# Performance work log

Measured on AMD Instinct MI355X. Metric: run time of the kernel, lower is better.

## Reference

```python
import jax, jax.numpy as jnp
import numpy as np
import math

MAX_VAL = 1e12
N = 1024        # max / actual seq len (l == n required by the module)
D = 512         # model dim
DK = 64         # head dim
H = D // DK     # 8 total heads
H_LOC = 4       # locker (local) heads
H_GLB = H - H_LOC


def setup_inputs() -> dict:
    key = jax.random.key(0)
    ks = jax.random.split(key, 10)
    b = 16
    inp = {
        "query": jax.random.normal(ks[0], (b, H, N, DK), jnp.float32),
        "key": jax.random.normal(ks[1], (b, H, N, DK), jnp.float32),
        "value": jax.random.normal(ks[2], (b, H, N, DK), jnp.float32),
        "mask": jax.random.randint(ks[3], (b, 1, N, N), 0, 2, jnp.int32),
        "users": jax.random.normal(ks[4], (b, N, D), jnp.float32),
        # learned params
        "rel_pos_table": jax.random.normal(ks[5], (2 * N - 1, H_LOC * DK), jnp.float32) * 0.02,
        "user_proj_w": jax.random.normal(ks[6], (D, H_LOC * DK), jnp.float32) * 0.02,
        "user_proj_b": jnp.zeros((H_LOC * DK,), jnp.float32),
        "mlp_w": jax.random.normal(ks[7], (H_LOC, DK), jnp.float32) * 0.1,
        "mlp_b": jnp.zeros((H_LOC,), jnp.float32),
    }
    return inp


def reference(query, key, value, mask, users, rel_pos_table, user_proj_w, user_proj_b, mlp_w, mlp_b):
    b, h, l, d_k = query.shape
    scale = 1.0 / math.sqrt(d_k)
    mask0 = (mask == 0)

    # ---- global heads: plain softmax attention ----
    q_g, k_g, v_g = query[:, :H_GLB], key[:, :H_GLB], value[:, :H_GLB]
    scores_g = jnp.einsum('bhqd,bhkd->bhqk', q_g, k_g) * scale
    scores_g = jnp.where(mask0, -MAX_VAL, scores_g)
    p_attn_g = jax.nn.softmax(scores_g, axis=-1)
    out_g = jnp.einsum('bhqk,bhkd->bhqd', p_attn_g, v_g)

    # ---- local (locker) heads: scores + per-head linear reweight ----
    q_l, k_l, v_l = query[:, H_GLB:], key[:, H_GLB:], value[:, H_GLB:]
    scores_l = jnp.einsum('bhqd,bhkd->bhqk', q_l, k_l) * scale

    # distance matrix and relative-position embedding, [h,q,k,d]
    distance = jnp.arange(l)[None, :] - jnp.arange(l)[:, None] + N - 1
    rel = rel_pos_table[distance].reshape(l, l, H_LOC, d_k).transpose(2, 0, 1, 3)

    # user projection -> [b,h,q,d]
    u = (users @ user_proj_w + user_proj_b).reshape(b, l, H_LOC, d_k).transpose(0, 2, 1, 3)

    # per-head Linear(d_k,1) applied to (rel + v_q + v_k + u_q); linearity lets us
    # distribute the dot product instead of materializing the [b,h,l,l,d_k] tensor.
    rw_rel = jnp.einsum('hqkd,hd->hqk', rel, mlp_w)[None]          # [1,h,q,k]
    rw_vq = jnp.einsum('bhqd,hd->bhq', v_l, mlp_w)[..., None]      # [b,h,q,1]
    rw_vk = jnp.einsum('bhkd,hd->bhk', v_l, mlp_w)[:, :, None, :]  # [b,h,1,k]
    rw_u = jnp.einsum('bhqd,hd->bhq', u, mlp_w)[..., None]         # [b,h,q,1]
    reweight = rw_rel + rw_vq + rw_vk + rw_u + mlp_b[None, :, None, None]

    scores_l = scores_l + reweight
    scores_l = jnp.where(mask0, -MAX_VAL, scores_l)
    p_attn_l = jax.nn.softmax(scores_l, axis=-1)
    out_l = jnp.einsum('bhqk,bhkd->bhqd', p_attn_l, v_l)

    out = jnp.concatenate([out_g, out_l], axis=1)
    return (out, p_attn_g, p_attn_l)
```

## Files before the change

kernel.cpp:

```cpp
#include <hip/hip_runtime.h>
#include <math.h>

#define NTOK 1024
#define SCALE 0.125f

#define WS_TREL   0
#define WS_RWV    8192
#define WS_RWU    73728
#define WS_W2     139264
#define WS_B2     141312

#define PG_OFF   8388608
#define PL_OFF   75497472

__global__ void prep0(const float* __restrict__ upw, const float* __restrict__ upb,
                      const float* __restrict__ mlw, const float* __restrict__ mlb,
                      const float* __restrict__ rpt, float* __restrict__ ws) {
    int gid = blockIdx.x * 256 + threadIdx.x;
    if (gid < 2048) {
        int c = gid >> 2, hl = gid & 3;
        const float* wrow = upw + c * 256 + hl * 64;
        const float* m = mlw + hl * 64;
        float acc = 0.f;
        #pragma unroll 8
        for (int d = 0; d < 64; ++d) acc += wrow[d] * m[d];
        ws[WS_W2 + gid] = acc;
    } else if (gid < 2052) {
        int hl = gid - 2048;
        const float* m = mlw + hl * 64;
        float acc = mlb[hl];
        #pragma unroll 8
        for (int d = 0; d < 64; ++d) acc += upb[hl * 64 + d] * m[d];
        ws[WS_B2 + hl] = acc;
    } else if (gid < 2052 + 2047 * 4) {
        int tt = gid - 2052;
        int dist = tt >> 2, hl = tt & 3;
        const float* r = rpt + dist * 256 + hl * 64;
        const float* m = mlw + hl * 64;
        float acc = 0.f;
        #pragma unroll 8
        for (int d = 0; d < 64; ++d) acc += r[d] * m[d];
        ws[WS_TREL + hl * 2048 + dist] = acc;
    }
}

__global__ void prep1(const float* __restrict__ value, const float* __restrict__ users,
                      const float* __restrict__ mlw, float* __restrict__ ws) {
    int t = threadIdx.x;
    int lane = t & 63, w = t >> 6;
    if (blockIdx.x < 256) {
        int wave = blockIdx.x * 4 + w;
        for (int r = 0; r < 64; ++r) {
            int row = wave * 64 + r;
            int b = row >> 12, hl = (row >> 10) & 3, n = row & 1023;
            float v = value[(((b * 8) + 4 + hl) * 1024 + n) * 64 + lane] * mlw[hl * 64 + lane];
            for (int m = 32; m; m >>= 1) v += __shfl_xor(v, m, 64);
            if (lane == 0) ws[WS_RWV + row] = v;
        }
    } else {
        __shared__ float w2[2052];
        for (int i = t; i < 2052; i += 256) w2[i] = ws[WS_W2 + i];
        __syncthreads();
        int wave = (blockIdx.x - 256) * 4 + w;
        for (int r = 0; r < 64; ++r) {
            int row = wave * 64 + r;
            int b = row >> 10, q = row & 1023;
            const float* ur = users + (b * 1024 + q) * 512;
            float p0 = 0.f, p1 = 0.f, p2 = 0.f, p3 = 0.f;
            #pragma unroll
            for (int j = 0; j < 8; ++j) {
                float uu = ur[lane + 64 * j];
                const float* wr = &w2[(lane + 64 * j) * 4];
                p0 += uu * wr[0]; p1 += uu * wr[1]; p2 += uu * wr[2]; p3 += uu * wr[3];
            }
            for (int m = 32; m; m >>= 1) {
                p0 += __shfl_xor(p0, m, 64); p1 += __shfl_xor(p1, m, 64);
                p2 += __shfl_xor(p2, m, 64); p3 += __shfl_xor(p3, m, 64);
            }
            if (lane == 0) {
                ws[WS_RWU + (b * 4 + 0) * 1024 + q] = p0 + w2[2048];
                ws[WS_RWU + (b * 4 + 1) * 1024 + q] = p1 + w2[2049];
                ws[WS_RWU + (b * 4 + 2) * 1024 + q] = p2 + w2[2050];
                ws[WS_RWU + (b * 4 + 3) * 1024 + q] = p3 + w2[2051];
            }
        }
    }
}

__launch_bounds__(256, 2)
__global__ void attn_main(const float* __restrict__ Q, const float* __restrict__ K,
                          const float* __restrict__ V, const int* __restrict__ mask,
                          const float* __restrict__ ws, float* __restrict__ out) {
    __shared__ float QT_s[64 * 128];
    __shared__ float SB[128 * 64];

    const int t = threadIdx.x;
    const int lbid = (blockIdx.x & 7) * 128 + (blockIdx.x >> 3);
    const int b = lbid >> 6, h = (lbid >> 3) & 7, qt = lbid & 7;
    const int q0 = qt * 128;
    const int qg = t >> 4, kg = t & 15;
    const bool loc = (h >= 4);
    const int hl = loc ? (h - 4) : 0;

    const float* Qb = Q + ((b * 8 + h) * 1024 + q0) * 64;
    const float* Kb = K + ((b * 8 + h) * 1024) * 64;
    const float* Vb = V + ((b * 8 + h) * 1024) * 64;
    const int*   Mb = mask + (b * 1024 + q0) * 1024;
    float* Pb = out + (loc ? (PL_OFF + ((b * 4 + hl) * 1024 + q0) * 1024)
                           : (PG_OFF + ((b * 4 + h ) * 1024 + q0) * 1024));
    float* Ob = out + ((b * 8 + h) * 1024 + q0) * 64;
    const float* rwv  = ws + WS_RWV + (b * 4 + hl) * 1024;
    const float* trel = ws + WS_TREL + hl * 2048;

    {
        int qr = t >> 1, d0 = 32 * (t & 1);
        const float* src = Qb + qr * 64 + d0;
        #pragma unroll
        for (int i = 0; i < 8; ++i) {
            float4 vv = *(const float4*)(src + 4 * i);
            QT_s[(d0 + 4 * i + 0) * 128 + qr] = vv.x;
            QT_s[(d0 + 4 * i + 1) * 128 + qr] = vv.y;
            QT_s[(d0 + 4 * i + 2) * 128 + qr] = vv.z;
            QT_s[(d0 + 4 * i + 3) * 128 + qr] = vv.w;
        }
    }
    float rq_r[8];
    #pragma unroll
    for (int i = 0; i < 8; ++i) rq_r[i] = 0.f;
    if (loc) {
        #pragma unroll
        for (int i = 0; i < 8; ++i) {
            int qq = 8 * qg + i;
            rq_r[i] = ws[WS_RWV + (b * 4 + hl) * 1024 + q0 + qq]
                    + ws[WS_RWU + (b * 4 + hl) * 1024 + q0 + qq];
        }
    }

    float o_[8][4];
    #pragma unroll
    for (int i = 0; i < 8; ++i)
        #pragma unroll
        for (int j = 0; j < 4; ++j) o_[i][j] = 0.f;
    float rs[8];
    #pragma unroll
    for (int i = 0; i < 8; ++i) rs[i] = 0.f;

    for (int s = 0; s < 8; ++s) {
        const int k0 = s * 128;
        __syncthreads();
        {
            int kr = t >> 1, d0 = 32 * (t & 1);
            const float* src = Kb + (k0 + kr) * 64 + d0;
            #pragma unroll
            for (int i = 0; i < 8; ++i) {
                float4 vv = *(const float4*)(src + 4 * i);
                SB[(d0 + 4 * i + 0) * 128 + kr] = vv.x;
                SB[(d0 + 4 * i + 1) * 128 + kr] = vv.y;
                SB[(d0 + 4 * i + 2) * 128 + kr] = vv.z;
                SB[(d0 + 4 * i + 3) * 128 + kr] = vv.w;
            }
        }
        __syncthreads();
        float c_[8][8];
        #pragma unroll
        for (int i = 0; i < 8; ++i)
            #pragma unroll
            for (int j = 0; j < 8; ++j) c_[i][j] = 0.f;
        #pragma unroll 4
        for (int d = 0; d < 64; ++d) {
            float4 a0 = *(const float4*)&QT_s[d * 128 + 8 * qg];
            float4 a1 = *(const float4*)&QT_s[d * 128 + 8 * qg + 4];
            float4 b0 = *(const float4*)&SB[d * 128 + 8 * kg];
            float4 b1 = *(const float4*)&SB[d * 128 + 8 * kg + 4];
            float aa[8] = {a0.x, a0.y, a0.z, a0.w, a1.x, a1.y, a1.z, a1.w};
            float bb[8] = {b0.x, b0.y, b0.z, b0.w, b1.x, b1.y, b1.z, b1.w};
            #pragma unroll
            for (int i = 0; i < 8; ++i)
                #pragma unroll
                for (int j = 0; j < 8; ++j)
                    c_[i][j] = fmaf(aa[i], bb[j], c_[i][j]);
        }
        float rvv[8];
        #pragma unroll
        for (int j = 0; j < 8; ++j) rvv[j] = 0.f;
        if (loc) {
            float4 rv0 = *(const float4*)(rwv + k0 + 8 * kg);
            float4 rv1 = *(const float4*)(rwv + k0 + 8 * kg + 4);
            rvv[0] = rv0.x; rvv[1] = rv0.y; rvv[2] = rv0.z; rvv[3] = rv0.w;
            rvv[4] = rv1.x; rvv[5] = rv1.y; rvv[6] = rv1.z; rvv[7] = rv1.w;
        }
        #pragma unroll
        for (int i = 0; i < 8; ++i) {
            int qq = 8 * qg + i;
            const int* mrow = Mb + qq * 1024 + k0 + 8 * kg;
            int4 m0 = *(const int4*)mrow;
            int4 m1 = *(const int4*)(mrow + 4);
            int mm[8] = {m0.x, m0.y, m0.z, m0.w, m1.x, m1.y, m1.z, m1.w};
            float tadd[8];
            if (loc) {
                const float* tb = trel + 1023 + k0 + 8 * kg - (q0 + qq);
                #pragma unroll
                for (int j = 0; j < 8; ++j) tadd[j] = rq_r[i] + tb[j] + rvv[j];
            } else {
                #pragma unroll
                for (int j = 0; j < 8; ++j) tadd[j] = 0.f;
            }
            float u[8];
            #pragma unroll
            for (int j = 0; j < 8; ++j) {
                float sc = fmaf(c_[i][j], SCALE, tadd[j]);
                u[j] = (mm[j] != 0) ? __expf(sc) : 0.f;
            }
            rs[i] += ((u[0] + u[1]) + (u[2] + u[3])) + ((u[4] + u[5]) + (u[6] + u[7]));
            float* prow = Pb + qq * 1024 + k0 + 8 * kg;
            *(float4*)prow       = make_float4(u[0], u[1], u[2], u[3]);
            *(float4*)(prow + 4) = make_float4(u[4], u[5], u[6], u[7]);
        }
        __syncthreads();
        {
            int kr = t >> 1, d0 = 32 * (t & 1);
            const float* src = Vb + (k0 + kr) * 64 + d0;
            #pragma unroll
            for (int i = 0; i < 8; ++i) {
                float4 vv = *(const float4*)(src + 4 * i);
                int cc = (d0 >> 2) + i;
                int ccs = cc ^ (kr & 7);
                *(float4*)&SB[kr * 64 + 4 * ccs] = vv;
            }
        }
        __syncthreads();
        #pragma unroll 2
        for (int kk = 0; kk < 128; kk += 4) {
            float4 v0 = *(const float4*)&SB[(kk + 0) * 64 + 4 * (kg ^ ((kk + 0) & 7))];
            float4 v1 = *(const float4*)&SB[(kk + 1) * 64 + 4 * (kg ^ ((kk + 1) & 7))];
            float4 v2 = *(const float4*)&SB[(kk + 2) * 64 + 4 * (kg ^ ((kk + 2) & 7))];
            float4 v3 = *(const float4*)&SB[(kk + 3) * 64 + 4 * (kg ^ ((kk + 3) & 7))];
            #pragma unroll
            for (int i = 0; i < 8; ++i) {
                float4 uu = *(const float4*)(Pb + (8 * qg + i) * 1024 + k0 + kk);
                o_[i][0] = fmaf(uu.x, v0.x, fmaf(uu.y, v1.x, fmaf(uu.z, v2.x, fmaf(uu.w, v3.x, o_[i][0]))));
                o_[i][1] = fmaf(uu.x, v0.y, fmaf(uu.y, v1.y, fmaf(uu.z, v2.y, fmaf(uu.w, v3.y, o_[i][1]))));
                o_[i][2] = fmaf(uu.x, v0.z, fmaf(uu.y, v1.z, fmaf(uu.z, v2.z, fmaf(uu.w, v3.z, o_[i][2]))));
                o_[i][3] = fmaf(uu.x, v0.w, fmaf(uu.y, v1.w, fmaf(uu.z, v2.w, fmaf(uu.w, v3.w, o_[i][3]))));
            }
        }
    }
    __syncthreads();
    #pragma unroll
    for (int i = 0; i < 8; ++i) {
        float v = rs[i];
        v += __shfl_xor(v, 1, 16); v += __shfl_xor(v, 2, 16);
        v += __shfl_xor(v, 4, 16); v += __shfl_xor(v, 8, 16);
        if (kg == 0) SB[8 * qg + i] = v;
    }
    __syncthreads();
    if (t < 128) {
        float sm = SB[t];
        SB[t]       = (sm > 0.f) ? (1.f / sm) : 0.f;
        SB[128 + t] = (sm > 0.f) ? 0.f : (1.f / 1024.f);
    }
    __syncthreads();
    for (int it = 0; it < 128; ++it) {
        float inv = SB[it], add = SB[128 + it];
        float4* pp = (float4*)(Pb + it * 1024) + t;
        float4 uu = *pp;
        uu.x = fmaf(uu.x, inv, add); uu.y = fmaf(uu.y, inv, add);
        uu.z = fmaf(uu.z, inv, add); uu.w = fmaf(uu.w, inv, add);
        *pp = uu;
    }
    #pragma unroll
    for (int i = 0; i < 8; ++i) {
        int qq = 8 * qg + i;
        float inv = SB[qq];
        *(float4*)(Ob + qq * 64 + 4 * kg) =
            make_float4(o_[i][0] * inv, o_[i][1] * inv, o_[i][2] * inv, o_[i][3] * inv);
    }
}

extern "C" void kernel_launch(void* const* d_in, const int* in_sizes, int n_in,
                              void* d_out, int out_size, void* d_ws, size_t ws_size,
                              hipStream_t stream) {
    (void)in_sizes; (void)n_in; (void)out_size; (void)ws_size;
    const float* q     = (const float*)d_in[0];
    const float* k     = (const float*)d_in[1];
    const float* v     = (const float*)d_in[2];
    const int*   mask  = (const int*)  d_in[3];
    const float* users = (const float*)d_in[4];
    const float* rpt   = (const float*)d_in[5];
    const float* upw   = (const float*)d_in[6];
    const float* upb   = (const float*)d_in[7];
    const float* mlw   = (const float*)d_in[8];
    const float* mlb   = (const float*)d_in[9];
    float* ws  = (float*)d_ws;
    float* out = (float*)d_out;

    hipLaunchKernelGGL(prep0, dim3(40),   dim3(256), 0, stream, upw, upb, mlw, mlb, rpt, ws);
    hipLaunchKernelGGL(prep1, dim3(320),  dim3(256), 0, stream, v, users, mlw, ws);
    hipLaunchKernelGGL(attn_main, dim3(1024), dim3(256), 0, stream, q, k, v, mask, ws, out);
}
```

Measured before the change: 1.630 ms.

## Rewrite attention as two-pass MFMA kernel with bitpacked mask and split-bf16 QK

Replaces the scalar-FMA attention kernel with a two-pass design. Pass one computes row sums and pass two recomputes scores, writes normalized probabilities once with nontemporal stores, and does P@V on MFMA. QK^T uses a hi/lo bf16 split (three MFMAs) to keep near-fp32 accuracy, while V and P are rounded to bf16 for the PV product. The int mask is pre-packed into 64-bit bitmasks by a new kernel, and log2e is folded into the precomputed biases so exp2 can be used. This removes the read-modify-write of the large probability tensor at the cost of computing QK^T twice and lower PV precision.

```diff
diff --git a/kernel.cpp b/kernel.cpp
--- a/kernel.cpp
+++ b/kernel.cpp
@@ -1,17 +1,21 @@
 #include <hip/hip_runtime.h>
 #include <math.h>
 
-#define NTOK 1024
-#define SCALE 0.125f
-
-#define WS_TREL   0
-#define WS_RWV    8192
-#define WS_RWU    73728
-#define WS_W2     139264
-#define WS_B2     141312
-
-#define PG_OFF   8388608
-#define PL_OFF   75497472
+#define L2E  1.4426950408889634f
+#define QSC  (0.125f * L2E)
+
+typedef float  f32x4 __attribute__((ext_vector_type(4)));
+typedef short  s16x8 __attribute__((ext_vector_type(8)));
+
+#define WS_TREL 0
+#define WS_RWV  8192
+#define WS_RWU  73728
+#define WS_W2   139264
+#define WS_B2   141312
+#define WS_PM   141320
+
+#define PG_OFF 8388608
+#define PL_OFF 75497472
 
 __global__ void prep0(const float* __restrict__ upw, const float* __restrict__ upb,
                       const float* __restrict__ mlw, const float* __restrict__ mlb,
@@ -40,7 +44,7 @@
         float acc = 0.f;
         #pragma unroll 8
         for (int d = 0; d < 64; ++d) acc += r[d] * m[d];
-        ws[WS_TREL + hl * 2048 + dist] = acc;
+        ws[WS_TREL + hl * 2048 + dist] = acc * L2E;
     }
 }
 
@@ -55,7 +59,7 @@
             int b = row >> 12, hl = (row >> 10) & 3, n = row & 1023;
             float v = value[(((b * 8) + 4 + hl) * 1024 + n) * 64 + lane] * mlw[hl * 64 + lane];
             for (int m = 32; m; m >>= 1) v += __shfl_xor(v, m, 64);
-            if (lane == 0) ws[WS_RWV + row] = v;
+            if (lane == 0) ws[WS_RWV + row] = v * L2E;
         }
     } else {
         __shared__ float w2[2052];
@@ -78,203 +82,285 @@
                 p2 += __shfl_xor(p2, m, 64); p3 += __shfl_xor(p3, m, 64);
             }
             if (lane == 0) {
-                ws[WS_RWU + (b * 4 + 0) * 1024 + q] = p0 + w2[2048];
-                ws[WS_RWU + (b * 4 + 1) * 1024 + q] = p1 + w2[2049];
-                ws[WS_RWU + (b * 4 + 2) * 1024 + q] = p2 + w2[2050];
-                ws[WS_RWU + (b * 4 + 3) * 1024 + q] = p3 + w2[2051];
-            }
-        }
-    }
-}
-
-__launch_bounds__(256, 2)
-__global__ void attn_main(const float* __restrict__ Q, const float* __restrict__ K,
-                          const float* __restrict__ V, const int* __restrict__ mask,
-                          const float* __restrict__ ws, float* __restrict__ out) {
-    __shared__ float QT_s[64 * 128];
-    __shared__ float SB[128 * 64];
+                ws[WS_RWU + (b * 4 + 0) * 1024 + q] = (p0 + w2[2048]) * L2E;
+                ws[WS_RWU + (b * 4 + 1) * 1024 + q] = (p1 + w2[2049]) * L2E;
+                ws[WS_RWU + (b * 4 + 2) * 1024 + q] = (p2 + w2[2050]) * L2E;
+                ws[WS_RWU + (b * 4 + 3) * 1024 + q] = (p3 + w2[2051]) * L2E;
+            }
+        }
+    }
+}
+
+__global__ void packm(const int* __restrict__ mask, unsigned long long* __restrict__ pm) {
+    int t = threadIdx.x, lane = t & 63, w = t >> 6;
+    int blk = blockIdx.x;
+    for (int i = w; i < 256; i += 4) {
+        int row = blk * 16 + (i >> 4);
+        int seg = i & 15;
+        int v = mask[row * 1024 + seg * 64 + lane];
+        unsigned long long bits = __ballot(v != 0);
+        if (lane == 0) pm[row * 16 + seg] = bits;
+    }
+}
+
+__device__ __forceinline__ int lswz(int row, int chunk) {
+    return (((chunk ^ (row & 7)) + (row >> 3)) & 7);
+}
+__device__ __forceinline__ s16x8 ldsfrag(const short* base, int row, int chunk) {
+    const char* p = (const char*)base + row * 144 + lswz(row, chunk) * 16;
+    return *(const s16x8*)p;
+}
+
+__launch_bounds__(256, 3)
+__global__ void attn_fused(const float* __restrict__ Q, const float* __restrict__ K,
+                           const float* __restrict__ V, const float* __restrict__ ws,
+                           float* __restrict__ out) {
+    __shared__ __align__(16) short BufKhi[64 * 72];
+    __shared__ __align__(16) short BufKlo[64 * 72];
+    __shared__ __align__(16) short BufV [64 * 72];
+    __shared__ __align__(16) short BufP [128 * 72];
 
     const int t = threadIdx.x;
     const int lbid = (blockIdx.x & 7) * 128 + (blockIdx.x >> 3);
     const int b = lbid >> 6, h = (lbid >> 3) & 7, qt = lbid & 7;
     const int q0 = qt * 128;
-    const int qg = t >> 4, kg = t & 15;
+    const int l = t & 63, n16 = l & 15, g = l >> 4;
+    const int wq0 = (t >> 6) * 32;
     const bool loc = (h >= 4);
-    const int hl = loc ? (h - 4) : 0;
+    const int hl = loc ? h - 4 : 0;
 
     const float* Qb = Q + ((b * 8 + h) * 1024 + q0) * 64;
     const float* Kb = K + ((b * 8 + h) * 1024) * 64;
     const float* Vb = V + ((b * 8 + h) * 1024) * 64;
-    const int*   Mb = mask + (b * 1024 + q0) * 1024;
+    const unsigned long long* pm =
+        ((const unsigned long long*)(ws + WS_PM)) + (size_t)b * 1024 * 16;
+    const float* trel = ws + WS_TREL + hl * 2048;
+    const float* rwvk = ws + WS_RWV + (b * 4 + hl) * 1024;
+    const float* rwuq = ws + WS_RWU + (b * 4 + hl) * 1024;
+
+    s16x8 qh[2][2], ql[2][2];
+    #pragma unroll
+    for (int mt = 0; mt < 2; ++mt)
+      #pragma unroll
+      for (int kc = 0; kc < 2; ++kc) {
+        const float* qp = Qb + (wq0 + mt * 16 + n16) * 64 + kc * 32 + g * 8;
+        float4 a = *(const float4*)qp;
+        float4 c = *(const float4*)(qp + 4);
+        float xs[8] = {a.x, a.y, a.z, a.w, c.x, c.y, c.z, c.w};
+        s16x8 vh, vl;
+        #pragma unroll
+        for (int e = 0; e < 8; ++e) {
+            float x = xs[e] * QSC;
+            unsigned u = __float_as_uint(x);
+            vh[e] = (short)(u >> 16);
+            float hf = __uint_as_float(u & 0xFFFF0000u);
+            vl[e] = (short)(__float_as_uint(x - hf) >> 16);
+        }
+        qh[mt][kc] = vh; ql[mt][kc] = vl;
+      }
+
+    float rq[2][4];
+    #pragma unroll
+    for (int mt = 0; mt < 2; ++mt)
+      #pragma unroll
+      for (int r = 0; r < 4; ++r) {
+        int qg = q0 + wq0 + mt * 16 + g * 4 + r;
+        rq[mt][r] = loc ? (rwvk[qg] + rwuq[qg]) : 0.f;
+      }
+
+    float rs[2][4] = {{0.f,0.f,0.f,0.f},{0.f,0.f,0.f,0.f}};
+    for (int s = 0; s < 16; ++s) {
+        const int k0 = s * 64;
+        __syncthreads();
+        #pragma unroll
+        for (int it = 0; it < 4; ++it) {
+            int kr = (t >> 4) + it * 16;
+            int d0 = (t & 15) * 4;
+            float4 kv = *(const float4*)(Kb + (k0 + kr) * 64 + d0);
+            float xk[4] = {kv.x, kv.y, kv.z, kv.w};
+            unsigned hh[4], llo[4];
+            #pragma unroll
+            for (int e = 0; e < 4; ++e) {
+                unsigned u = __float_as_uint(xk[e]);
+                hh[e] = u >> 16;
+                float hf = __uint_as_float(u & 0xFFFF0000u);
+                llo[e] = __float_as_uint(xk[e] - hf) >> 16;
+            }
+            uint2 wh = make_uint2(hh[0] | (hh[1] << 16), hh[2] | (hh[3] << 16));
+            uint2 wl = make_uint2(llo[0] | (llo[1] << 16), llo[2] | (llo[3] << 16));
+            int off = kr * 144 + lswz(kr, d0 >> 3) * 16 + (d0 & 7) * 2;
+            *(uint2*)((char*)BufKhi + off) = wh;
+            *(uint2*)((char*)BufKlo + off) = wl;
+        }
+        __syncthreads();
+
+        f32x4 acc[2][4];
+        #pragma unroll
+        for (int mt = 0; mt < 2; ++mt)
+          #pragma unroll
+          for (int nt = 0; nt < 4; ++nt) acc[mt][nt] = (f32x4){0.f,0.f,0.f,0.f};
+        #pragma unroll
+        for (int kc = 0; kc < 2; ++kc)
+          #pragma unroll
+          for (int nt = 0; nt < 4; ++nt) {
+            s16x8 kh = ldsfrag(BufKhi, nt * 16 + n16, kc * 4 + g);
+            s16x8 kl = ldsfrag(BufKlo, nt * 16 + n16, kc * 4 + g);
+            #pragma unroll
+            for (int mt = 0; mt < 2; ++mt) {
+                acc[mt][nt] = __builtin_amdgcn_mfma_f32_16x16x32_bf16(qh[mt][kc], kh, acc[mt][nt], 0, 0, 0);
+                acc[mt][nt] = __builtin_amdgcn_mfma_f32_16x16x32_bf16(qh[mt][kc], kl, acc[mt][nt], 0, 0, 0);
+                acc[mt][nt] = __builtin_amdgcn_mfma_f32_16x16x32_bf16(ql[mt][kc], kh, acc[mt][nt], 0, 0, 0);
+            }
+          }
+
+        float rvv[4] = {0.f,0.f,0.f,0.f};
+        if (loc) {
+            #pragma unroll
+            for (int nt = 0; nt < 4; ++nt) rvv[nt] = rwvk[k0 + nt * 16 + n16];
+        }
+        #pragma unroll
+        for (int mt = 0; mt < 2; ++mt)
+          #pragma unroll
+          for (int r = 0; r < 4; ++r) {
+            int qg = q0 + wq0 + mt * 16 + g * 4 + r;
+            unsigned long long mb = pm[qg * 16 + s];
+            const float* tb = trel + 1023 + k0 - qg;
+            #pragma unroll
+            for (int nt = 0; nt < 4; ++nt) {
+                float sc = acc[mt][nt][r] + rq[mt][r];
+                if (loc) sc += tb[nt * 16 + n16] + rvv[nt];
+                float u = ((mb >> (nt * 16 + n16)) & 1ULL) ? exp2f(sc) : 0.f;
+                rs[mt][r] += u;
+            }
+          }
+    }
+
+    float inv_[2][4];
+    #pragma unroll
+    for (int mt = 0; mt < 2; ++mt)
+      #pragma unroll
+      for (int r = 0; r < 4; ++r) {
+        float v = rs[mt][r];
+        v += __shfl_xor(v, 1); v += __shfl_xor(v, 2);
+        v += __shfl_xor(v, 4); v += __shfl_xor(v, 8);
+        inv_[mt][r] = (v > 0.f) ? (1.f / v) : -1.f;
+      }
+
+    f32x4 o_[2][4];
+    #pragma unroll
+    for (int mt = 0; mt < 2; ++mt)
+      #pragma unroll
+      for (int dt = 0; dt < 4; ++dt) o_[mt][dt] = (f32x4){0.f,0.f,0.f,0.f};
+
     float* Pb = out + (loc ? (PL_OFF + ((b * 4 + hl) * 1024 + q0) * 1024)
                            : (PG_OFF + ((b * 4 + h ) * 1024 + q0) * 1024));
+
+    for (int s = 0; s < 16; ++s) {
+        const int k0 = s * 64;
+        __syncthreads();
+        #pragma unroll
+        for (int it = 0; it < 4; ++it) {
+            int kr = (t >> 4) + it * 16;
+            int d0 = (t & 15) * 4;
+            float4 kv = *(const float4*)(Kb + (k0 + kr) * 64 + d0);
+            float xk[4] = {kv.x, kv.y, kv.z, kv.w};
+            unsigned hh[4], llo[4];
+            #pragma unroll
+            for (int e = 0; e < 4; ++e) {
+                unsigned u = __float_as_uint(xk[e]);
+                hh[e] = u >> 16;
+                float hf = __uint_as_float(u & 0xFFFF0000u);
+                llo[e] = __float_as_uint(xk[e] - hf) >> 16;
+            }
+            uint2 wh = make_uint2(hh[0] | (hh[1] << 16), hh[2] | (hh[3] << 16));
+            uint2 wl = make_uint2(llo[0] | (llo[1] << 16), llo[2] | (llo[3] << 16));
+            int off = kr * 144 + lswz(kr, d0 >> 3) * 16 + (d0 & 7) * 2;
+            *(uint2*)((char*)BufKhi + off) = wh;
+            *(uint2*)((char*)BufKlo + off) = wl;
+            float4 vv = *(const float4*)(Vb + (k0 + kr) * 64 + d0);
+            float xv[4] = {vv.x, vv.y, vv.z, vv.w};
+            #pragma unroll
+            for (int e = 0; e < 4; ++e) {
+                unsigned u = __float_as_uint(xv[e]);
+                unsigned rr = u + 0x7FFFu + ((u >> 16) & 1u);
+                int d = d0 + e;
+                *(short*)((char*)BufV + d * 144 + lswz(d, kr >> 3) * 16 + (kr & 7) * 2) =
+                    (short)(rr >> 16);
+            }
+        }
+        __syncthreads();
+
+        f32x4 acc[2][4];
+        #pragma unroll
+        for (int mt = 0; mt < 2; ++mt)
+          #pragma unroll
+          for (int nt = 0; nt < 4; ++nt) acc[mt][nt] = (f32x4){0.f,0.f,0.f,0.f};
+        #pragma unroll
+        for (int kc = 0; kc < 2; ++kc)
+          #pragma unroll
+          for (int nt = 0; nt < 4; ++nt) {
+            s16x8 kh = ldsfrag(BufKhi, nt * 16 + n16, kc * 4 + g);
+            s16x8 kl = ldsfrag(BufKlo, nt * 16 + n16, kc * 4 + g);
+            #pragma unroll
+            for (int mt = 0; mt < 2; ++mt) {
+                acc[mt][nt] = __builtin_amdgcn_mfma_f32_16x16x32_bf16(qh[mt][kc], kh, acc[mt][nt], 0, 0, 0);
+                acc[mt][nt] = __builtin_amdgcn_mfma_f32_16x16x32_bf16(qh[mt][kc], kl, acc[mt][nt], 0, 0, 0);
+                acc[mt][nt] = __builtin_amdgcn_mfma_f32_16x16x32_bf16(ql[mt][kc], kh, acc[mt][nt], 0, 0, 0);
+            }
+          }
+
+        float rvv[4] = {0.f,0.f,0.f,0.f};
+        if (loc) {
+            #pragma unroll
+            for (int nt = 0; nt < 4; ++nt) rvv[nt] = rwvk[k0 + nt * 16 + n16];
+        }
+        #pragma unroll
+        for (int mt = 0; mt < 2; ++mt)
+          #pragma unroll
+          for (int r = 0; r < 4; ++r) {
+            int qloc = wq0 + mt * 16 + g * 4 + r;
+            int qg = q0 + qloc;
+            unsigned long long mb = pm[qg * 16 + s];
+            const float* tb = trel + 1023 + k0 - qg;
+            float iv = inv_[mt][r];
+            #pragma unroll
+            for (int nt = 0; nt < 4; ++nt) {
+                float sc = acc[mt][nt][r] + rq[mt][r];
+                if (loc) sc += tb[nt * 16 + n16] + rvv[nt];
+                float u = ((mb >> (nt * 16 + n16)) & 1ULL) ? exp2f(sc) : 0.f;
+                float p = (iv > 0.f) ? u * iv : (1.f / 1024.f);
+                __builtin_nontemporal_store(p, Pb + qloc * 1024 + k0 + nt * 16 + n16);
+                unsigned uu = __float_as_uint(p);
+                unsigned rr = uu + 0x7FFFu + ((uu >> 16) & 1u);
+                int kl_ = nt * 16 + n16;
+                *(short*)((char*)BufP + qloc * 144 + lswz(qloc, kl_ >> 3) * 16 + (kl_ & 7) * 2) =
+                    (short)(rr >> 16);
+            }
+          }
+
+        #pragma unroll
+        for (int kc = 0; kc < 2; ++kc) {
+            s16x8 pa0 = ldsfrag(BufP, wq0 + n16,      kc * 4 + g);
+            s16x8 pa1 = ldsfrag(BufP, wq0 + 16 + n16, kc * 4 + g);
+            #pragma unroll
+            for (int dt = 0; dt < 4; ++dt) {
+                s16x8 vb = ldsfrag(BufV, dt * 16 + n16, kc * 4 + g);
+                o_[0][dt] = __builtin_amdgcn_mfma_f32_16x16x32_bf16(pa0, vb, o_[0][dt], 0, 0, 0);
+                o_[1][dt] = __builtin_amdgcn_mfma_f32_16x16x32_bf16(pa1, vb, o_[1][dt], 0, 0, 0);
+            }
+        }
+    }
+
     float* Ob = out + ((b * 8 + h) * 1024 + q0) * 64;
-    const float* rwv  = ws + WS_RWV + (b * 4 + hl) * 1024;
-    const float* trel = ws + WS_TREL + hl * 2048;
-
-    {
-        int qr = t >> 1, d0 = 32 * (t & 1);
-        const float* src = Qb + qr * 64 + d0;
-        #pragma unroll
-        for (int i = 0; i < 8; ++i) {
-            float4 vv = *(const float4*)(src + 4 * i);
-            QT_s[(d0 + 4 * i + 0) * 128 + qr] = vv.x;
-            QT_s[(d0 + 4 * i + 1) * 128 + qr] = vv.y;
-            QT_s[(d0 + 4 * i + 2) * 128 + qr] = vv.z;
-            QT_s[(d0 + 4 * i + 3) * 128 + qr] = vv.w;
-        }
-    }
-    float rq_r[8];
-    #pragma unroll
-    for (int i = 0; i < 8; ++i) rq_r[i] = 0.f;
-    if (loc) {
-        #pragma unroll
-        for (int i = 0; i < 8; ++i) {
-            int qq = 8 * qg + i;
-            rq_r[i] = ws[WS_RWV + (b * 4 + hl) * 1024 + q0 + qq]
-                    + ws[WS_RWU + (b * 4 + hl) * 1024 + q0 + qq];
-        }
-    }
-
-    float o_[8][4];
-    #pragma unroll
-    for (int i = 0; i < 8; ++i)
-        #pragma unroll
-        for (int j = 0; j < 4; ++j) o_[i][j] = 0.f;
-    float rs[8];
-    #pragma unroll
-    for (int i = 0; i < 8; ++i) rs[i] = 0.f;
-
-    for (int s = 0; s < 8; ++s) {
-        const int k0 = s * 128;
-        __syncthreads();
-        {
-            int kr = t >> 1, d0 = 32 * (t & 1);
-            const float* src = Kb + (k0 + kr) * 64 + d0;
-            #pragma unroll
-            for (int i = 0; i < 8; ++i) {
-                float4 vv = *(const float4*)(src + 4 * i);
-                SB[(d0 + 4 * i + 0) * 128 + kr] = vv.x;
-                SB[(d0 + 4 * i + 1) * 128 + kr] = vv.y;
-                SB[(d0 + 4 * i + 2) * 128 + kr] = vv.z;
-                SB[(d0 + 4 * i + 3) * 128 + kr] = vv.w;
-            }
-        }
-        __syncthreads();
-        float c_[8][8];
-        #pragma unroll
-        for (int i = 0; i < 8; ++i)
-            #pragma unroll
-            for (int j = 0; j < 8; ++j) c_[i][j] = 0.f;
-        #pragma unroll 4
-        for (int d = 0; d < 64; ++d) {
-            float4 a0 = *(const float4*)&QT_s[d * 128 + 8 * qg];
-            float4 a1 = *(const float4*)&QT_s[d * 128 + 8 * qg + 4];
-            float4 b0 = *(const float4*)&SB[d * 128 + 8 * kg];
-            float4 b1 = *(const float4*)&SB[d * 128 + 8 * kg + 4];
-            float aa[8] = {a0.x, a0.y, a0.z, a0.w, a1.x, a1.y, a1.z, a1.w};
-            float bb[8] = {b0.x, b0.y, b0.z, b0.w, b1.x, b1.y, b1.z, b1.w};
-            #pragma unroll
-            for (int i = 0; i < 8; ++i)
-                #pragma unroll
-                for (int j = 0; j < 8; ++j)
-                    c_[i][j] = fmaf(aa[i], bb[j], c_[i][j]);
-        }
-        float rvv[8];
-        #pragma unroll
-        for (int j = 0; j < 8; ++j) rvv[j] = 0.f;
-        if (loc) {
-            float4 rv0 = *(const float4*)(rwv + k0 + 8 * kg);
-            float4 rv1 = *(const float4*)(rwv + k0 + 8 * kg + 4);
-            rvv[0] = rv0.x; rvv[1] = rv0.y; rvv[2] = rv0.z; rvv[3] = rv0.w;
-            rvv[4] = rv1.x; rvv[5] = rv1.y; rvv[6] = rv1.z; rvv[7] = rv1.w;
-        }
-        #pragma unroll
-        for (int i = 0; i < 8; ++i) {
-            int qq = 8 * qg + i;
-            const int* mrow = Mb + qq * 1024 + k0 + 8 * kg;
-            int4 m0 = *(const int4*)mrow;
-            int4 m1 = *(const int4*)(mrow + 4);
-            int mm[8] = {m0.x, m0.y, m0.z, m0.w, m1.x, m1.y, m1.z, m1.w};
-            float tadd[8];
-            if (loc) {
-                const float* tb = trel + 1023 + k0 + 8 * kg - (q0 + qq);
-                #pragma unroll
-                for (int j = 0; j < 8; ++j) tadd[j] = rq_r[i] + tb[j] + rvv[j];
-            } else {
-                #pragma unroll
-                for (int j = 0; j < 8; ++j) tadd[j] = 0.f;
-            }
-            float u[8];
-            #pragma unroll
-            for (int j = 0; j < 8; ++j) {
-                float sc = fmaf(c_[i][j], SCALE, tadd[j]);
-                u[j] = (mm[j] != 0) ? __expf(sc) : 0.f;
-            }
-            rs[i] += ((u[0] + u[1]) + (u[2] + u[3])) + ((u[4] + u[5]) + (u[6] + u[7]));
-            float* prow = Pb + qq * 1024 + k0 + 8 * kg;
-            *(float4*)prow       = make_float4(u[0], u[1], u[2], u[3]);
-            *(float4*)(prow + 4) = make_float4(u[4], u[5], u[6], u[7]);
-        }
-        __syncthreads();
-        {
-            int kr = t >> 1, d0 = 32 * (t & 1);
-            const float* src = Vb + (k0 + kr) * 64 + d0;
-            #pragma unroll
-            for (int i = 0; i < 8; ++i) {
-                float4 vv = *(const float4*)(src + 4 * i);
-                int cc = (d0 >> 2) + i;
-                int ccs = cc ^ (kr & 7);
-                *(float4*)&SB[kr * 64 + 4 * ccs] = vv;
-            }
-        }
-        __syncthreads();
-        #pragma unroll 2
-        for (int kk = 0; kk < 128; kk += 4) {
-            float4 v0 = *(const float4*)&SB[(kk + 0) * 64 + 4 * (kg ^ ((kk + 0) & 7))];
-            float4 v1 = *(const float4*)&SB[(kk + 1) * 64 + 4 * (kg ^ ((kk + 1) & 7))];
-            float4 v2 = *(const float4*)&SB[(kk + 2) * 64 + 4 * (kg ^ ((kk + 2) & 7))];
-            float4 v3 = *(const float4*)&SB[(kk + 3) * 64 + 4 * (kg ^ ((kk + 3) & 7))];
-            #pragma unroll
-            for (int i = 0; i < 8; ++i) {
-                float4 uu = *(const float4*)(Pb + (8 * qg + i) * 1024 + k0 + kk);
-                o_[i][0] = fmaf(uu.x, v0.x, fmaf(uu.y, v1.x, fmaf(uu.z, v2.x, fmaf(uu.w, v3.x, o_[i][0]))));
-                o_[i][1] = fmaf(uu.x, v0.y, fmaf(uu.y, v1.y, fmaf(uu.z, v2.y, fmaf(uu.w, v3.y, o_[i][1]))));
-                o_[i][2] = fmaf(uu.x, v0.z, fmaf(uu.y, v1.z, fmaf(uu.z, v2.z, fmaf(uu.w, v3.z, o_[i][2]))));
-                o_[i][3] = fmaf(uu.x, v0.w, fmaf(uu.y, v1.w, fmaf(uu.z, v2.w, fmaf(uu.w, v3.w, o_[i][3]))));
-            }
-        }
-    }
-    __syncthreads();
-    #pragma unroll
-    for (int i = 0; i < 8; ++i) {
-        float v = rs[i];
-        v += __shfl_xor(v, 1, 16); v += __shfl_xor(v, 2, 16);
-        v += __shfl_xor(v, 4, 16); v += __shfl_xor(v, 8, 16);
-        if (kg == 0) SB[8 * qg + i] = v;
-    }
-    __syncthreads();
-    if (t < 128) {
-        float sm = SB[t];
-        SB[t]       = (sm > 0.f) ? (1.f / sm) : 0.f;
-        SB[128 + t] = (sm > 0.f) ? 0.f : (1.f / 1024.f);
-    }
-    __syncthreads();
-    for (int it = 0; it < 128; ++it) {
-        float inv = SB[it], add = SB[128 + it];
-        float4* pp = (float4*)(Pb + it * 1024) + t;
-        float4 uu = *pp;
-        uu.x = fmaf(uu.x, inv, add); uu.y = fmaf(uu.y, inv, add);
-        uu.z = fmaf(uu.z, inv, add); uu.w = fmaf(uu.w, inv, add);
-        *pp = uu;
-    }
-    #pragma unroll
-    for (int i = 0; i < 8; ++i) {
-        int qq = 8 * qg + i;
-        float inv = SB[qq];
-        *(float4*)(Ob + qq * 64 + 4 * kg) =
-            make_float4(o_[i][0] * inv, o_[i][1] * inv, o_[i][2] * inv, o_[i][3] * inv);
-    }
+    #pragma unroll
+    for (int mt = 0; mt < 2; ++mt)
+      #pragma unroll
+      for (int dt = 0; dt < 4; ++dt)
+        #pragma unroll
+        for (int r = 0; r < 4; ++r) {
+            int qloc = wq0 + mt * 16 + g * 4 + r;
+            __builtin_nontemporal_store(o_[mt][dt][r], Ob + qloc * 64 + dt * 16 + n16);
+        }
 }
 
 extern "C" void kernel_launch(void* const* d_in, const int* in_sizes, int n_in,
@@ -296,5 +382,7 @@
 
     hipLaunchKernelGGL(prep0, dim3(40),   dim3(256), 0, stream, upw, upb, mlw, mlb, rpt, ws);
     hipLaunchKernelGGL(prep1, dim3(320),  dim3(256), 0, stream, v, users, mlw, ws);
-    hipLaunchKernelGGL(attn_main, dim3(1024), dim3(256), 0, stream, q, k, v, mask, ws, out);
-}
+    hipLaunchKernelGGL(packm, dim3(1024), dim3(256), 0, stream, mask,
+                       (unsigned long long*)(ws + WS_PM));
+    hipLaunchKernelGGL(attn_fused, dim3(1024), dim3(256), 0, stream, q, k, v, ws, out);
+}
```

Result: faster. 1.559 ms (-4.4%).
